# Optimization experiments

Measured on AMD Instinct MI355X. Metric: run time of the kernel, lower is better.

## Reference

```python
import jax, jax.numpy as jnp
import numpy as np
from jax import lax

V, E, H, L, T, B = 50000, 512, 1024, 2, 512, 64


def _lstm_layer(x_seq, h0, c0, W_ih, W_hh):
    # x_seq: [T, B, D_in]; W_ih: [4H, D_in]; W_hh: [4H, H]
    x_proj = jnp.einsum('tbd,gd->tbg', x_seq, W_ih)  # precompute input projection

    def step(carry, xp):
        h, c = carry
        gates = xp + h @ W_hh.T  # [B, 4H], PyTorch gate order i,f,g,o
        i, f, g, o = jnp.split(gates, 4, axis=-1)
        i = jax.nn.sigmoid(i)
        f = jax.nn.sigmoid(f)
        g = jnp.tanh(g)
        o = jax.nn.sigmoid(o)
        c = f * c + i * g
        h = o * jnp.tanh(c)
        return (h, c), h

    (hT, cT), ys = lax.scan(step, (h0, c0), x_proj)
    return ys, hT, cT


def setup_inputs() -> dict:
    key = jax.random.key(0)
    ks = jax.random.split(key, 8)
    inputs = jax.random.randint(ks[0], (T, B), 0, V)
    h0 = jnp.zeros((L, B, H), jnp.float32)
    c0 = jnp.zeros((L, B, H), jnp.float32)
    emb = jax.random.uniform(ks[1], (V, E), jnp.float32, -0.1, 0.1)
    s_ih0 = 1.0 / np.sqrt(H)
    W_ih0 = jax.random.uniform(ks[2], (4 * H, E), jnp.float32, -s_ih0, s_ih0)
    W_hh0 = jax.random.uniform(ks[3], (4 * H, H), jnp.float32, -s_ih0, s_ih0)
    W_ih1 = jax.random.uniform(ks[4], (4 * H, H), jnp.float32, -s_ih0, s_ih0)
    W_hh1 = jax.random.uniform(ks[5], (4 * H, H), jnp.float32, -s_ih0, s_ih0)
    dec_W = jax.random.uniform(ks[6], (1, H), jnp.float32, -0.1, 0.1)
    dec_b = jnp.zeros((1,), jnp.float32)
    return {"inputs": inputs, "h0": h0, "c0": c0, "emb": emb,
            "W_ih0": W_ih0, "W_hh0": W_hh0, "W_ih1": W_ih1, "W_hh1": W_hh1,
            "dec_W": dec_W, "dec_b": dec_b}


def reference(inputs, h0, c0, emb, W_ih0, W_hh0, W_ih1, W_hh1, dec_W, dec_b):
    x = emb[inputs]                                      # [T, B, E]
    y0, h1, c1 = _lstm_layer(x, h0[0], c0[0], W_ih0, W_hh0)   # [T, B, H]
    # dropout between layers is inference-disabled (eval mode)
    y1, h2, c2 = _lstm_layer(y0, h0[1], c0[1], W_ih1, W_hh1)  # [T, B, H]
    pooled = jnp.mean(y1, axis=0)                        # [B, H] (squeeze is a no-op)
    decoded = pooled @ dec_W.T + dec_b                   # [B, 1]
    hn = jnp.stack([h1, h2])
    cn = jnp.stack([c1, c2])
    return decoded, hn, cn
```

## Files before the change

kernel.cpp:

```cpp
#include <hip/hip_runtime.h>

#define TT 512
#define BB 64
#define HH 1024
#define EE 512
#define VV 50000
#define BBHH (BB*HH)
#define BPL 128
#define NBLK 256

typedef __attribute__((ext_vector_type(8))) short bf16x8;
typedef __attribute__((ext_vector_type(4))) float f32x4;

__device__ inline unsigned short f2b(float f){
  unsigned int u; __builtin_memcpy(&u, &f, 4);
  unsigned int r = (u + 0x7FFFu + ((u >> 16) & 1u)) >> 16;
  return (unsigned short)r;
}
__device__ inline float sigmoidf_(float x){ return 1.0f / (1.0f + __expf(-x)); }
__device__ inline float tanhf_(float x){ float e = __expf(2.0f * x); return 1.0f - 2.0f / (e + 1.0f); }

__device__ inline bf16x8 pack8(float4 a, float4 b){
  bf16x8 r;
  r[0] = (short)f2b(a.x); r[1] = (short)f2b(a.y); r[2] = (short)f2b(a.z); r[3] = (short)f2b(a.w);
  r[4] = (short)f2b(b.x); r[5] = (short)f2b(b.y); r[6] = (short)f2b(b.z); r[7] = (short)f2b(b.w);
  return r;
}

__global__ void cast_f2b(const float* __restrict__ src, unsigned short* __restrict__ dst, long n){
  long i = ((long)blockIdx.x * blockDim.x + threadIdx.x) * 4;
  long stride = (long)gridDim.x * blockDim.x * 4;
  for (; i + 3 < n; i += stride){
    float4 v = *reinterpret_cast<const float4*>(src + i);
    ushort4 r;
    r.x = f2b(v.x); r.y = f2b(v.y); r.z = f2b(v.z); r.w = f2b(v.w);
    *reinterpret_cast<ushort4*>(dst + i) = r;
  }
}

__global__ void init_h(const float* __restrict__ h0,
                       unsigned short* __restrict__ h0ic, unsigned short* __restrict__ h1ic){
  int i = blockIdx.x * blockDim.x + threadIdx.x;
  int b = i >> 10, j = i & (HH - 1);
  int d = (((j >> 3) * BB) + b) * 8 + (j & 7);
  h0ic[d] = f2b(h0[i]);
  h1ic[d] = f2b(h0[BBHH + i]);
}

__device__ __forceinline__ void wait_layer(const unsigned* __restrict__ f, unsigned e, int lane){
  unsigned a = __hip_atomic_load(f + lane,      __ATOMIC_RELAXED, __HIP_MEMORY_SCOPE_AGENT);
  unsigned b = __hip_atomic_load(f + 64 + lane, __ATOMIC_RELAXED, __HIP_MEMORY_SCOPE_AGENT);
  while (!__all(a >= e && b >= e)){
    __builtin_amdgcn_s_sleep(8);
    a = __hip_atomic_load(f + lane,      __ATOMIC_RELAXED, __HIP_MEMORY_SCOPE_AGENT);
    b = __hip_atomic_load(f + 64 + lane, __ATOMIC_RELAXED, __HIP_MEMORY_SCOPE_AGENT);
  }
}

__device__ __forceinline__ void publish(unsigned* __restrict__ f, int bid_l, unsigned e){
  asm volatile("s_waitcnt vmcnt(0)" ::: "memory");
  __syncthreads();
  if (threadIdx.x == 0)
    __hip_atomic_store(f + bid_l, e, __ATOMIC_RELAXED, __HIP_MEMORY_SCOPE_AGENT);
}

#define LIDX(m, s) ((((m) * 16 + (s)) * 64 + lane) * 4)

#define CBASE ((wid * 32 + hi) * (BB * 8) + l16 * 8)

__device__ void run_l0(
    int bid_l, int lane, int wid, int l16, int hi, int kq,
    const int* __restrict__ inputs, const float* __restrict__ c0,
    const unsigned short* __restrict__ emb_bf,
    const float* __restrict__ Wih0, const float* __restrict__ Whh0,
    const unsigned short* __restrict__ h0ic,
    unsigned short* __restrict__ hist0,
    float* __restrict__ hn, float* __restrict__ cn,
    unsigned* __restrict__ flags0, float* lds)
{
  const int j0 = bid_l * 8;
  const int bown = wid * 16 + l16;
  const int cbase = CBASE;

  bf16x8 wx[2][4], wh[2][8];
  #pragma unroll
  for (int m = 0; m < 2; ++m){
    const int g = l16 & 3;
    const int u = 2 * (l16 >> 2) + m;
    const float* rx = Wih0 + (size_t)(g * HH + j0 + u) * EE;
    const float* rh = Whh0 + (size_t)(g * HH + j0 + u) * HH;
    #pragma unroll
    for (int kk = 0; kk < 4; ++kk){
      int k0 = wid * 128 + kk * 32 + kq;
      wx[m][kk] = pack8(*reinterpret_cast<const float4*>(rx + k0),
                        *reinterpret_cast<const float4*>(rx + k0 + 4));
    }
    #pragma unroll
    for (int kk = 0; kk < 8; ++kk){
      int k0 = wid * 256 + kk * 32 + kq;
      wh[m][kk] = pack8(*reinterpret_cast<const float4*>(rh + k0),
                        *reinterpret_cast<const float4*>(rh + k0 + 4));
    }
  }

  float cs[2];
  #pragma unroll
  for (int m = 0; m < 2; ++m)
    cs[m] = c0[(size_t)bown * HH + j0 + 2 * hi + m];

  for (int t = 0; t < TT; ++t){
    f32x4 acc[2][4];
    #pragma unroll
    for (int m = 0; m < 2; ++m)
      #pragma unroll
      for (int nt = 0; nt < 4; ++nt)
        acc[m][nt] = (f32x4){0.f,0.f,0.f,0.f};

    {
      const unsigned short* xr[4];
      #pragma unroll
      for (int nt = 0; nt < 4; ++nt)
        xr[nt] = emb_bf + (size_t)inputs[t * BB + nt * 16 + l16] * EE;
      #pragma unroll
      for (int kk = 0; kk < 4; ++kk){
        const int kb = wid * 128 + kk * 32 + kq;
        #pragma unroll
        for (int nt = 0; nt < 4; ++nt){
          bf16x8 bf = *reinterpret_cast<const bf16x8*>(xr[nt] + kb);
          acc[0][nt] = __builtin_amdgcn_mfma_f32_16x16x32_bf16(wx[0][kk], bf, acc[0][nt], 0, 0, 0);
          acc[1][nt] = __builtin_amdgcn_mfma_f32_16x16x32_bf16(wx[1][kk], bf, acc[1][nt], 0, 0, 0);
        }
      }
    }

    if (t > 0) wait_layer(flags0, (unsigned)t, lane);

    {
      const unsigned short* hs = (t == 0) ? h0ic : hist0 + (size_t)(t - 1) * BBHH;
      #pragma unroll
      for (int kk = 0; kk < 8; ++kk){
        #pragma unroll
        for (int nt = 0; nt < 4; ++nt){
          bf16x8 bf = *reinterpret_cast<const bf16x8*>(hs + cbase + kk * 2048 + nt * 128);
          acc[0][nt] = __builtin_amdgcn_mfma_f32_16x16x32_bf16(wh[0][kk], bf, acc[0][nt], 0, 0, 0);
          acc[1][nt] = __builtin_amdgcn_mfma_f32_16x16x32_bf16(wh[1][kk], bf, acc[1][nt], 0, 0, 0);
        }
      }
    }

    #pragma unroll
    for (int m = 0; m < 2; ++m)
      #pragma unroll
      for (int nt = 0; nt < 4; ++nt)
        *reinterpret_cast<f32x4*>(&lds[LIDX(m, wid * 4 + nt)]) = acc[m][nt];
    __syncthreads();
    f32x4 s[2];
    #pragma unroll
    for (int m = 0; m < 2; ++m){
      s[m] = (f32x4){0.f,0.f,0.f,0.f};
      #pragma unroll
      for (int w = 0; w < 4; ++w)
        s[m] += *reinterpret_cast<f32x4*>(&lds[LIDX(m, w * 4 + wid)]);
    }

    float hv[2];
    #pragma unroll
    for (int m = 0; m < 2; ++m){
      float gi = sigmoidf_(s[m][0]), gf = sigmoidf_(s[m][1]);
      float gg = tanhf_(s[m][2]),    go = sigmoidf_(s[m][3]);
      cs[m] = gf * cs[m] + gi * gg;
      hv[m] = go * tanhf_(cs[m]);
    }
    unsigned w = (unsigned)f2b(hv[0]) | ((unsigned)f2b(hv[1]) << 16);
    __hip_atomic_store(reinterpret_cast<unsigned*>(hist0 + (size_t)t * BBHH + (size_t)(bid_l * BB + bown) * 8 + 2 * hi),
                       w, __ATOMIC_RELAXED, __HIP_MEMORY_SCOPE_AGENT);
    if (t == TT - 1){
      size_t o = (size_t)bown * HH + j0 + 2 * hi;
      *reinterpret_cast<float2*>(hn + o) = make_float2(hv[0], hv[1]);
      *reinterpret_cast<float2*>(cn + o) = make_float2(cs[0], cs[1]);
    }

    publish(flags0, bid_l, (unsigned)(t + 1));
  }
}

__device__ void run_l1(
    int bid_l, int lane, int wid, int l16, int hi, int kq,
    const float* __restrict__ c0,
    const float* __restrict__ Wih1, const float* __restrict__ Whh1,
    const unsigned short* __restrict__ h1ic,
    const unsigned short* __restrict__ hist0, unsigned short* __restrict__ hist1,
    const float* __restrict__ decW, const float* __restrict__ decb,
    float* __restrict__ dec_out, float* __restrict__ hn, float* __restrict__ cn,
    unsigned* __restrict__ flags0, unsigned* __restrict__ flags1, float* lds)
{
  const int j0 = bid_l * 8;
  const int bown = wid * 16 + l16;
  const int cbase = CBASE;

  bf16x8 wx[2][8], wh[2][8];
  #pragma unroll
  for (int m = 0; m < 2; ++m){
    const int g = l16 & 3;
    const int u = 2 * (l16 >> 2) + m;
    const float* rx = Wih1 + (size_t)(g * HH + j0 + u) * HH;
    const float* rh = Whh1 + (size_t)(g * HH + j0 + u) * HH;
    #pragma unroll
    for (int kk = 0; kk < 8; ++kk){
      int k0 = wid * 256 + kk * 32 + kq;
      wx[m][kk] = pack8(*reinterpret_cast<const float4*>(rx + k0),
                        *reinterpret_cast<const float4*>(rx + k0 + 4));
      wh[m][kk] = pack8(*reinterpret_cast<const float4*>(rh + k0),
                        *reinterpret_cast<const float4*>(rh + k0 + 4));
    }
  }

  float cs[2];
  #pragma unroll
  for (int m = 0; m < 2; ++m)
    cs[m] = c0[(size_t)BBHH + (size_t)bown * HH + j0 + 2 * hi + m];
  float pooldec = 0.0f;
  const float dwv0 = decW[j0 + 2 * hi], dwv1 = decW[j0 + 2 * hi + 1];

  for (int t = 0; t < TT; ++t){
    f32x4 acc[2][4];
    #pragma unroll
    for (int m = 0; m < 2; ++m)
      #pragma unroll
      for (int nt = 0; nt < 4; ++nt)
        acc[m][nt] = (f32x4){0.f,0.f,0.f,0.f};

    if (t > 0) wait_layer(flags1, (unsigned)t, lane);
    {
      const unsigned short* hs = (t == 0) ? h1ic : hist1 + (size_t)(t - 1) * BBHH;
      #pragma unroll
      for (int kk = 0; kk < 8; ++kk){
        #pragma unroll
        for (int nt = 0; nt < 4; ++nt){
          bf16x8 bf = *reinterpret_cast<const bf16x8*>(hs + cbase + kk * 2048 + nt * 128);
          acc[0][nt] = __builtin_amdgcn_mfma_f32_16x16x32_bf16(wh[0][kk], bf, acc[0][nt], 0, 0, 0);
          acc[1][nt] = __builtin_amdgcn_mfma_f32_16x16x32_bf16(wh[1][kk], bf, acc[1][nt], 0, 0, 0);
        }
      }
    }

    wait_layer(flags0, (unsigned)(t + 1), lane);
    {
      const unsigned short* xs = hist0 + (size_t)t * BBHH;
      #pragma unroll
      for (int kk = 0; kk < 8; ++kk){
        #pragma unroll
        for (int nt = 0; nt < 4; ++nt){
          bf16x8 bf = *reinterpret_cast<const bf16x8*>(xs + cbase + kk * 2048 + nt * 128);
          acc[0][nt] = __builtin_amdgcn_mfma_f32_16x16x32_bf16(wx[0][kk], bf, acc[0][nt], 0, 0, 0);
          acc[1][nt] = __builtin_amdgcn_mfma_f32_16x16x32_bf16(wx[1][kk], bf, acc[1][nt], 0, 0, 0);
        }
      }
    }

    #pragma unroll
    for (int m = 0; m < 2; ++m)
      #pragma unroll
      for (int nt = 0; nt < 4; ++nt)
        *reinterpret_cast<f32x4*>(&lds[LIDX(m, wid * 4 + nt)]) = acc[m][nt];
    __syncthreads();
    f32x4 s[2];
    #pragma unroll
    for (int m = 0; m < 2; ++m){
      s[m] = (f32x4){0.f,0.f,0.f,0.f};
      #pragma unroll
      for (int w = 0; w < 4; ++w)
        s[m] += *reinterpret_cast<f32x4*>(&lds[LIDX(m, w * 4 + wid)]);
    }

    float hv[2];
    #pragma unroll
    for (int m = 0; m < 2; ++m){
      float gi = sigmoidf_(s[m][0]), gf = sigmoidf_(s[m][1]);
      float gg = tanhf_(s[m][2]),    go = sigmoidf_(s[m][3]);
      cs[m] = gf * cs[m] + gi * gg;
      hv[m] = go * tanhf_(cs[m]);
    }
    unsigned w = (unsigned)f2b(hv[0]) | ((unsigned)f2b(hv[1]) << 16);
    __hip_atomic_store(reinterpret_cast<unsigned*>(hist1 + (size_t)t * BBHH + (size_t)(bid_l * BB + bown) * 8 + 2 * hi),
                       w, __ATOMIC_RELAXED, __HIP_MEMORY_SCOPE_AGENT);
    pooldec += hv[0] * dwv0 + hv[1] * dwv1;
    if (t == TT - 1){
      size_t o = (size_t)BBHH + (size_t)bown * HH + j0 + 2 * hi;
      *reinterpret_cast<float2*>(hn + o) = make_float2(hv[0], hv[1]);
      *reinterpret_cast<float2*>(cn + o) = make_float2(cs[0], cs[1]);
    }

    publish(flags1, bid_l, (unsigned)(t + 1));
  }

  pooldec += __shfl_xor(pooldec, 16);
  pooldec += __shfl_xor(pooldec, 32);
  if (hi == 0){
    float contrib = pooldec * (1.0f / (float)TT);
    if (bid_l == 0) contrib += decb[0];
    atomicAdd(&dec_out[bown], contrib);
  }
}

__global__ __launch_bounds__(256, 1) void lstm_persist(
    const int* __restrict__ inputs, const float* __restrict__ c0,
    const unsigned short* __restrict__ emb_bf,
    const float* __restrict__ Wih0, const float* __restrict__ Whh0,
    const float* __restrict__ Wih1, const float* __restrict__ Whh1,
    const unsigned short* __restrict__ h0ic, const unsigned short* __restrict__ h1ic,
    unsigned short* __restrict__ hist0, unsigned short* __restrict__ hist1,
    const float* __restrict__ decW, const float* __restrict__ decb,
    float* __restrict__ dec_out, float* __restrict__ hn, float* __restrict__ cn,
    unsigned* __restrict__ flags)
{
  __shared__ float lds[2 * 16 * 64 * 4];
  const int tid  = threadIdx.x;
  const int lane = tid & 63;
  const int wid  = tid >> 6;
  const int l16  = lane & 15;
  const int hi   = lane >> 4;
  const int kq   = hi << 3;
  unsigned* flags0 = flags;
  unsigned* flags1 = flags + 128;

  int bid = blockIdx.x;
  if (bid < BPL){
    run_l0(bid, lane, wid, l16, hi, kq, inputs, c0, emb_bf, Wih0, Whh0,
           h0ic, hist0, hn, cn, flags0, lds);
  } else {
    run_l1(bid - BPL, lane, wid, l16, hi, kq, c0, Wih1, Whh1,
           h1ic, hist0, hist1, decW, decb, dec_out, hn, cn, flags0, flags1, lds);
  }
}

extern "C" void kernel_launch(void* const* d_in, const int* in_sizes, int n_in,
                              void* d_out, int out_size, void* d_ws, size_t ws_size,
                              hipStream_t stream){
  const int*   inputs = (const int*)d_in[0];
  const float* h0     = (const float*)d_in[1];
  const float* c0     = (const float*)d_in[2];
  const float* emb    = (const float*)d_in[3];
  const float* Wih0   = (const float*)d_in[4];
  const float* Whh0   = (const float*)d_in[5];
  const float* Wih1   = (const float*)d_in[6];
  const float* Whh1   = (const float*)d_in[7];
  const float* decW   = (const float*)d_in[8];
  const float* decb   = (const float*)d_in[9];

  char* ws = (char*)d_ws;
  size_t off = 0;
  auto alloc = [&](size_t bytes) -> void* {
    void* p = ws + off;
    off += (bytes + 255) & ~(size_t)255;
    return p;
  };
  unsigned short* emb_bf = (unsigned short*)alloc((size_t)VV * EE * 2);
  unsigned short* hist0  = (unsigned short*)alloc((size_t)TT * BBHH * 2);
  unsigned short* hist1  = (unsigned short*)alloc((size_t)TT * BBHH * 2);
  unsigned short* h0ic   = (unsigned short*)alloc((size_t)BBHH * 2);
  unsigned short* h1ic   = (unsigned short*)alloc((size_t)BBHH * 2);
  unsigned int*   flags  = (unsigned int*)alloc((size_t)256 * 4);

  float* out = (float*)d_out;
  float* hn  = out + BB;
  float* cn  = out + BB + 2 * BBHH;

  hipMemsetAsync(flags, 0, 256 * 4, stream);
  hipMemsetAsync(out, 0, BB * 4, stream);

  cast_f2b<<<2048, 256, 0, stream>>>(emb, emb_bf, (long)VV * EE);
  init_h<<<BBHH / 256, 256, 0, stream>>>(h0, h0ic, h1ic);

  lstm_persist<<<NBLK, 256, 0, stream>>>(inputs, c0, emb_bf,
                                         Wih0, Whh0, Wih1, Whh1,
                                         h0ic, h1ic, hist0, hist1,
                                         decW, decb, out, hn, cn, flags);
}
```

Baseline: 4.286 ms.

## Split batch across 8 waves and replace block barriers with LDS counters

Doubles each persistent block to 512 threads (8 waves), splitting the batch in half across wave pairs so each wave issues half as many MFMAs per step. Block-wide __syncthreads are replaced with LDS atomic counters and a single-wave global flag poll that releases the other waves through an LDS go-word. The cross-block publish becomes a last-arriver atomic increment, which aims to shorten the per-timestep critical path. In exchange there are more waves per CU, spin loops on LDS, and more complex memory-ordering reasoning that could be fragile.

```diff
diff --git a/kernel.cpp b/kernel.cpp
--- a/kernel.cpp
+++ b/kernel.cpp
@@ -11,35 +11,38 @@
 
 typedef __attribute__((ext_vector_type(8))) short bf16x8;
 typedef __attribute__((ext_vector_type(4))) float f32x4;
-
-__device__ inline unsigned short f2b(float f){
-  unsigned int u; __builtin_memcpy(&u, &f, 4);
-  unsigned int r = (u + 0x7FFFu + ((u >> 16) & 1u)) >> 16;
-  return (unsigned short)r;
+typedef unsigned short us;
+
+#define MFMA(a,b,c) __builtin_amdgcn_mfma_f32_16x16x32_bf16((a),(b),(c),0,0,0)
+#define LDG(p) __hip_atomic_load((p), __ATOMIC_RELAXED, __HIP_MEMORY_SCOPE_AGENT)
+#define ZIDX(ks,m,ntg,ln) (((((ks)*2+(m))*4+(ntg))*64+(ln))*4)
+
+__device__ inline us f2b(float f){
+  unsigned u; __builtin_memcpy(&u, &f, 4);
+  return (us)((u + 0x7FFFu + ((u >> 16) & 1u)) >> 16);
 }
 __device__ inline float sigmoidf_(float x){ return 1.0f / (1.0f + __expf(-x)); }
 __device__ inline float tanhf_(float x){ float e = __expf(2.0f * x); return 1.0f - 2.0f / (e + 1.0f); }
 
 __device__ inline bf16x8 pack8(float4 a, float4 b){
   bf16x8 r;
-  r[0] = (short)f2b(a.x); r[1] = (short)f2b(a.y); r[2] = (short)f2b(a.z); r[3] = (short)f2b(a.w);
-  r[4] = (short)f2b(b.x); r[5] = (short)f2b(b.y); r[6] = (short)f2b(b.z); r[7] = (short)f2b(b.w);
+  r[0]=(short)f2b(a.x); r[1]=(short)f2b(a.y); r[2]=(short)f2b(a.z); r[3]=(short)f2b(a.w);
+  r[4]=(short)f2b(b.x); r[5]=(short)f2b(b.y); r[6]=(short)f2b(b.z); r[7]=(short)f2b(b.w);
   return r;
 }
 
-__global__ void cast_f2b(const float* __restrict__ src, unsigned short* __restrict__ dst, long n){
+__global__ void cast_f2b(const float* __restrict__ src, us* __restrict__ dst, long n){
   long i = ((long)blockIdx.x * blockDim.x + threadIdx.x) * 4;
   long stride = (long)gridDim.x * blockDim.x * 4;
   for (; i + 3 < n; i += stride){
     float4 v = *reinterpret_cast<const float4*>(src + i);
-    ushort4 r;
-    r.x = f2b(v.x); r.y = f2b(v.y); r.z = f2b(v.z); r.w = f2b(v.w);
+    ushort4 r; r.x=f2b(v.x); r.y=f2b(v.y); r.z=f2b(v.z); r.w=f2b(v.w);
     *reinterpret_cast<ushort4*>(dst + i) = r;
   }
 }
 
 __global__ void init_h(const float* __restrict__ h0,
-                       unsigned short* __restrict__ h0ic, unsigned short* __restrict__ h1ic){
+                       us* __restrict__ h0ic, us* __restrict__ h1ic){
   int i = blockIdx.x * blockDim.x + threadIdx.x;
   int b = i >> 10, j = i & (HH - 1);
   int d = (((j >> 3) * BB) + b) * 8 + (j & 7);
@@ -47,290 +50,326 @@
   h1ic[d] = f2b(h0[BBHH + i]);
 }
 
-__device__ __forceinline__ void wait_layer(const unsigned* __restrict__ f, unsigned e, int lane){
-  unsigned a = __hip_atomic_load(f + lane,      __ATOMIC_RELAXED, __HIP_MEMORY_SCOPE_AGENT);
-  unsigned b = __hip_atomic_load(f + 64 + lane, __ATOMIC_RELAXED, __HIP_MEMORY_SCOPE_AGENT);
-  while (!__all(a >= e && b >= e)){
-    __builtin_amdgcn_s_sleep(8);
-    a = __hip_atomic_load(f + lane,      __ATOMIC_RELAXED, __HIP_MEMORY_SCOPE_AGENT);
-    b = __hip_atomic_load(f + 64 + lane, __ATOMIC_RELAXED, __HIP_MEMORY_SCOPE_AGENT);
-  }
-}
-
-__device__ __forceinline__ void publish(unsigned* __restrict__ f, int bid_l, unsigned e){
-  asm volatile("s_waitcnt vmcnt(0)" ::: "memory");
-  __syncthreads();
-  if (threadIdx.x == 0)
-    __hip_atomic_store(f + bid_l, e, __ATOMIC_RELAXED, __HIP_MEMORY_SCOPE_AGENT);
-}
-
-#define LIDX(m, s) ((((m) * 16 + (s)) * 64 + lane) * 4)
-
-#define CBASE ((wid * 32 + hi) * (BB * 8) + l16 * 8)
-
-__device__ void run_l0(
-    int bid_l, int lane, int wid, int l16, int hi, int kq,
-    const int* __restrict__ inputs, const float* __restrict__ c0,
-    const unsigned short* __restrict__ emb_bf,
-    const float* __restrict__ Wih0, const float* __restrict__ Whh0,
-    const unsigned short* __restrict__ h0ic,
-    unsigned short* __restrict__ hist0,
+__device__ __forceinline__ void poll_flags(const unsigned* f, unsigned e, int lane){
+  for(;;){
+    unsigned a = LDG(f + lane);
+    unsigned b = LDG(f + 64 + lane);
+    if (__all((int)(a >= e && b >= e))) break;
+    __builtin_amdgcn_s_sleep(1);
+  }
+}
+__device__ __forceinline__ void wave_gate(unsigned* go, unsigned gval,
+                                          const unsigned* f, unsigned e, int lane, int wid){
+  if (wid == 0){
+    poll_flags(f, e, lane);
+    __hip_atomic_store(go, gval, __ATOMIC_RELAXED, __HIP_MEMORY_SCOPE_WORKGROUP);
+  } else {
+    while (__hip_atomic_load(go, __ATOMIC_RELAXED, __HIP_MEMORY_SCOPE_WORKGROUP) < gval)
+      __builtin_amdgcn_s_sleep(1);
+  }
+}
+__device__ __forceinline__ void lds_spin(unsigned* c, unsigned tgt){
+  while (__hip_atomic_load(c, __ATOMIC_RELAXED, __HIP_MEMORY_SCOPE_WORKGROUP) < tgt)
+    __builtin_amdgcn_s_sleep(1);
+}
+
+__device__ void run_l0(int bid_l, const int* __restrict__ inputs, const float* __restrict__ c0,
+    const us* __restrict__ emb_bf, const float* __restrict__ Wih0, const float* __restrict__ Whh0,
+    const us* __restrict__ h0ic, us* __restrict__ hist0,
     float* __restrict__ hn, float* __restrict__ cn,
-    unsigned* __restrict__ flags0, float* lds)
+    unsigned* __restrict__ flags0,
+    float* zone, unsigned* ctrA, unsigned* ctrR, unsigned* ctrP, unsigned* go0)
 {
+  const int tid = threadIdx.x, lane = tid & 63, wid = tid >> 6;
+  const int l16 = lane & 15, hi = lane >> 4, kq = hi << 3;
+  const int ks = wid & 3, bh = wid >> 2;
   const int j0 = bid_l * 8;
-  const int bown = wid * 16 + l16;
-  const int cbase = CBASE;
 
   bf16x8 wx[2][4], wh[2][8];
   #pragma unroll
   for (int m = 0; m < 2; ++m){
-    const int g = l16 & 3;
-    const int u = 2 * (l16 >> 2) + m;
+    const int g = l16 & 3, u = 2 * (l16 >> 2) + m;
     const float* rx = Wih0 + (size_t)(g * HH + j0 + u) * EE;
     const float* rh = Whh0 + (size_t)(g * HH + j0 + u) * HH;
     #pragma unroll
     for (int kk = 0; kk < 4; ++kk){
-      int k0 = wid * 128 + kk * 32 + kq;
-      wx[m][kk] = pack8(*reinterpret_cast<const float4*>(rx + k0),
-                        *reinterpret_cast<const float4*>(rx + k0 + 4));
+      int k0 = ks * 128 + kk * 32 + kq;
+      wx[m][kk] = pack8(*(const float4*)(rx + k0), *(const float4*)(rx + k0 + 4));
     }
     #pragma unroll
     for (int kk = 0; kk < 8; ++kk){
-      int k0 = wid * 256 + kk * 32 + kq;
-      wh[m][kk] = pack8(*reinterpret_cast<const float4*>(rh + k0),
-                        *reinterpret_cast<const float4*>(rh + k0 + 4));
-    }
-  }
-
-  float cs[2];
-  #pragma unroll
-  for (int m = 0; m < 2; ++m)
-    cs[m] = c0[(size_t)bown * HH + j0 + 2 * hi + m];
+      int k0 = ks * 256 + kk * 32 + kq;
+      wh[m][kk] = pack8(*(const float4*)(rh + k0), *(const float4*)(rh + k0 + 4));
+    }
+  }
+
+  const int bown  = wid * 8 + (lane >> 2);
+  const int u0    = 2 * (lane & 3);
+  const int ntg_r = bown >> 4;
+  const int lam   = (lane & 3) * 16 + (bown & 15);
+  float cs0 = 0.f, cs1 = 0.f;
+  if (lane < 32){
+    cs0 = c0[(size_t)bown * HH + j0 + u0];
+    cs1 = c0[(size_t)bown * HH + j0 + u0 + 1];
+  }
 
   for (int t = 0; t < TT; ++t){
-    f32x4 acc[2][4];
+    f32x4 acc[2][2];
+    acc[0][0]=acc[0][1]=acc[1][0]=acc[1][1]=(f32x4){0.f,0.f,0.f,0.f};
+
+    {
+      const us* xr0 = emb_bf + (size_t)inputs[t*BB + bh*32 + l16] * EE;
+      const us* xr1 = emb_bf + (size_t)inputs[t*BB + bh*32 + 16 + l16] * EE;
+      #pragma unroll
+      for (int kk = 0; kk < 4; ++kk){
+        const int kb = ks * 128 + kk * 32 + kq;
+        bf16x8 b0 = *(const bf16x8*)(xr0 + kb);
+        bf16x8 b1 = *(const bf16x8*)(xr1 + kb);
+        acc[0][0] = MFMA(wx[0][kk], b0, acc[0][0]);
+        acc[1][0] = MFMA(wx[1][kk], b0, acc[1][0]);
+        acc[0][1] = MFMA(wx[0][kk], b1, acc[0][1]);
+        acc[1][1] = MFMA(wx[1][kk], b1, acc[1][1]);
+      }
+    }
+
+    if (t > 0){
+      asm volatile("s_waitcnt vmcnt(0)" ::: "memory");
+      if (lane == 0){
+        unsigned old = atomicAdd(ctrP, 1u);
+        if (old == 8u * (unsigned)t - 1u)
+          __hip_atomic_store(flags0 + bid_l, (unsigned)t, __ATOMIC_RELAXED, __HIP_MEMORY_SCOPE_AGENT);
+      }
+    }
+
+    if (t > 0) wave_gate(go0, (unsigned)t, flags0, (unsigned)t, lane, wid);
+
+    {
+      const us* hs = (t == 0) ? h0ic : hist0 + (size_t)(t - 1) * BBHH;
+      #pragma unroll
+      for (int kk = 0; kk < 8; ++kk){
+        const us* p = hs + (size_t)(ks * 32 + kk * 4 + hi) * 512;
+        bf16x8 b0 = *(const bf16x8*)(p + (bh*32 + l16) * 8);
+        bf16x8 b1 = *(const bf16x8*)(p + (bh*32 + 16 + l16) * 8);
+        acc[0][0] = MFMA(wh[0][kk], b0, acc[0][0]);
+        acc[1][0] = MFMA(wh[1][kk], b0, acc[1][0]);
+        acc[0][1] = MFMA(wh[0][kk], b1, acc[0][1]);
+        acc[1][1] = MFMA(wh[1][kk], b1, acc[1][1]);
+      }
+    }
+
+    if (t > 0) lds_spin(ctrR, 8u * (unsigned)t);
+
     #pragma unroll
     for (int m = 0; m < 2; ++m)
       #pragma unroll
-      for (int nt = 0; nt < 4; ++nt)
-        acc[m][nt] = (f32x4){0.f,0.f,0.f,0.f};
-
-    {
-      const unsigned short* xr[4];
-      #pragma unroll
-      for (int nt = 0; nt < 4; ++nt)
-        xr[nt] = emb_bf + (size_t)inputs[t * BB + nt * 16 + l16] * EE;
-      #pragma unroll
-      for (int kk = 0; kk < 4; ++kk){
-        const int kb = wid * 128 + kk * 32 + kq;
-        #pragma unroll
-        for (int nt = 0; nt < 4; ++nt){
-          bf16x8 bf = *reinterpret_cast<const bf16x8*>(xr[nt] + kb);
-          acc[0][nt] = __builtin_amdgcn_mfma_f32_16x16x32_bf16(wx[0][kk], bf, acc[0][nt], 0, 0, 0);
-          acc[1][nt] = __builtin_amdgcn_mfma_f32_16x16x32_bf16(wx[1][kk], bf, acc[1][nt], 0, 0, 0);
-        }
-      }
-    }
-
-    if (t > 0) wait_layer(flags0, (unsigned)t, lane);
-
-    {
-      const unsigned short* hs = (t == 0) ? h0ic : hist0 + (size_t)(t - 1) * BBHH;
-      #pragma unroll
-      for (int kk = 0; kk < 8; ++kk){
-        #pragma unroll
-        for (int nt = 0; nt < 4; ++nt){
-          bf16x8 bf = *reinterpret_cast<const bf16x8*>(hs + cbase + kk * 2048 + nt * 128);
-          acc[0][nt] = __builtin_amdgcn_mfma_f32_16x16x32_bf16(wh[0][kk], bf, acc[0][nt], 0, 0, 0);
-          acc[1][nt] = __builtin_amdgcn_mfma_f32_16x16x32_bf16(wh[1][kk], bf, acc[1][nt], 0, 0, 0);
-        }
-      }
-    }
-
-    #pragma unroll
-    for (int m = 0; m < 2; ++m)
-      #pragma unroll
-      for (int nt = 0; nt < 4; ++nt)
-        *reinterpret_cast<f32x4*>(&lds[LIDX(m, wid * 4 + nt)]) = acc[m][nt];
-    __syncthreads();
-    f32x4 s[2];
-    #pragma unroll
-    for (int m = 0; m < 2; ++m){
-      s[m] = (f32x4){0.f,0.f,0.f,0.f};
-      #pragma unroll
-      for (int w = 0; w < 4; ++w)
-        s[m] += *reinterpret_cast<f32x4*>(&lds[LIDX(m, w * 4 + wid)]);
-    }
-
-    float hv[2];
-    #pragma unroll
-    for (int m = 0; m < 2; ++m){
-      float gi = sigmoidf_(s[m][0]), gf = sigmoidf_(s[m][1]);
-      float gg = tanhf_(s[m][2]),    go = sigmoidf_(s[m][3]);
-      cs[m] = gf * cs[m] + gi * gg;
-      hv[m] = go * tanhf_(cs[m]);
-    }
-    unsigned w = (unsigned)f2b(hv[0]) | ((unsigned)f2b(hv[1]) << 16);
-    __hip_atomic_store(reinterpret_cast<unsigned*>(hist0 + (size_t)t * BBHH + (size_t)(bid_l * BB + bown) * 8 + 2 * hi),
-                       w, __ATOMIC_RELAXED, __HIP_MEMORY_SCOPE_AGENT);
-    if (t == TT - 1){
-      size_t o = (size_t)bown * HH + j0 + 2 * hi;
-      *reinterpret_cast<float2*>(hn + o) = make_float2(hv[0], hv[1]);
-      *reinterpret_cast<float2*>(cn + o) = make_float2(cs[0], cs[1]);
-    }
-
-    publish(flags0, bid_l, (unsigned)(t + 1));
-  }
-}
-
-__device__ void run_l1(
-    int bid_l, int lane, int wid, int l16, int hi, int kq,
-    const float* __restrict__ c0,
+      for (int ntl = 0; ntl < 2; ++ntl)
+        *(f32x4*)&zone[ZIDX(ks, m, bh*2 + ntl, lane)] = acc[m][ntl];
+    asm volatile("s_waitcnt lgkmcnt(0)" ::: "memory");
+    if (lane == 0) atomicAdd(ctrA, 1u);
+    lds_spin(ctrA, 8u * (unsigned)(t + 1));
+
+    if (lane < 32){
+      f32x4 s0 = (f32x4){0.f,0.f,0.f,0.f}, s1 = (f32x4){0.f,0.f,0.f,0.f};
+      #pragma unroll
+      for (int kr = 0; kr < 4; ++kr){
+        s0 += *(f32x4*)&zone[ZIDX(kr, 0, ntg_r, lam)];
+        s1 += *(f32x4*)&zone[ZIDX(kr, 1, ntg_r, lam)];
+      }
+      float gi = sigmoidf_(s0[0]), gf = sigmoidf_(s0[1]);
+      float gg = tanhf_(s0[2]),    go = sigmoidf_(s0[3]);
+      cs0 = gf * cs0 + gi * gg;
+      float hv0 = go * tanhf_(cs0);
+      gi = sigmoidf_(s1[0]); gf = sigmoidf_(s1[1]);
+      gg = tanhf_(s1[2]);    go = sigmoidf_(s1[3]);
+      cs1 = gf * cs1 + gi * gg;
+      float hv1 = go * tanhf_(cs1);
+
+      unsigned w = (unsigned)f2b(hv0) | ((unsigned)f2b(hv1) << 16);
+      __hip_atomic_store((unsigned*)(hist0 + (size_t)t * BBHH + ((size_t)(bid_l*64 + bown))*8 + u0),
+                         w, __ATOMIC_RELAXED, __HIP_MEMORY_SCOPE_AGENT);
+      if (t == TT - 1){
+        size_t o = (size_t)bown * HH + j0 + u0;
+        *reinterpret_cast<float2*>(hn + o) = make_float2(hv0, hv1);
+        *reinterpret_cast<float2*>(cn + o) = make_float2(cs0, cs1);
+      }
+    }
+    asm volatile("s_waitcnt lgkmcnt(0)" ::: "memory");
+    if (lane == 0) atomicAdd(ctrR, 1u);
+  }
+
+  asm volatile("s_waitcnt vmcnt(0)" ::: "memory");
+  if (lane == 0){
+    unsigned old = atomicAdd(ctrP, 1u);
+    if (old == 8u * (unsigned)TT - 1u)
+      __hip_atomic_store(flags0 + bid_l, (unsigned)TT, __ATOMIC_RELAXED, __HIP_MEMORY_SCOPE_AGENT);
+  }
+}
+
+__device__ void run_l1(int bid_l, const float* __restrict__ c0,
     const float* __restrict__ Wih1, const float* __restrict__ Whh1,
-    const unsigned short* __restrict__ h1ic,
-    const unsigned short* __restrict__ hist0, unsigned short* __restrict__ hist1,
+    const us* __restrict__ h1ic, const us* __restrict__ hist0, us* __restrict__ hist1,
     const float* __restrict__ decW, const float* __restrict__ decb,
     float* __restrict__ dec_out, float* __restrict__ hn, float* __restrict__ cn,
-    unsigned* __restrict__ flags0, unsigned* __restrict__ flags1, float* lds)
+    unsigned* __restrict__ flags0, unsigned* __restrict__ flags1,
+    float* zone, unsigned* ctrA, unsigned* ctrR, unsigned* ctrP,
+    unsigned* go1, unsigned* go2)
 {
+  const int tid = threadIdx.x, lane = tid & 63, wid = tid >> 6;
+  const int l16 = lane & 15, hi = lane >> 4, kq = hi << 3;
+  const int ks = wid & 3, bh = wid >> 2;
   const int j0 = bid_l * 8;
-  const int bown = wid * 16 + l16;
-  const int cbase = CBASE;
 
   bf16x8 wx[2][8], wh[2][8];
   #pragma unroll
   for (int m = 0; m < 2; ++m){
-    const int g = l16 & 3;
-    const int u = 2 * (l16 >> 2) + m;
+    const int g = l16 & 3, u = 2 * (l16 >> 2) + m;
     const float* rx = Wih1 + (size_t)(g * HH + j0 + u) * HH;
     const float* rh = Whh1 + (size_t)(g * HH + j0 + u) * HH;
     #pragma unroll
     for (int kk = 0; kk < 8; ++kk){
-      int k0 = wid * 256 + kk * 32 + kq;
-      wx[m][kk] = pack8(*reinterpret_cast<const float4*>(rx + k0),
-                        *reinterpret_cast<const float4*>(rx + k0 + 4));
-      wh[m][kk] = pack8(*reinterpret_cast<const float4*>(rh + k0),
-                        *reinterpret_cast<const float4*>(rh + k0 + 4));
-    }
-  }
-
-  float cs[2];
-  #pragma unroll
-  for (int m = 0; m < 2; ++m)
-    cs[m] = c0[(size_t)BBHH + (size_t)bown * HH + j0 + 2 * hi + m];
-  float pooldec = 0.0f;
-  const float dwv0 = decW[j0 + 2 * hi], dwv1 = decW[j0 + 2 * hi + 1];
+      int k0 = ks * 256 + kk * 32 + kq;
+      wx[m][kk] = pack8(*(const float4*)(rx + k0), *(const float4*)(rx + k0 + 4));
+      wh[m][kk] = pack8(*(const float4*)(rh + k0), *(const float4*)(rh + k0 + 4));
+    }
+  }
+
+  const int bown  = wid * 8 + (lane >> 2);
+  const int u0    = 2 * (lane & 3);
+  const int ntg_r = bown >> 4;
+  const int lam   = (lane & 3) * 16 + (bown & 15);
+  float cs0 = 0.f, cs1 = 0.f, pooldec = 0.f, dw0 = 0.f, dw1 = 0.f;
+  if (lane < 32){
+    cs0 = c0[(size_t)BBHH + (size_t)bown * HH + j0 + u0];
+    cs1 = c0[(size_t)BBHH + (size_t)bown * HH + j0 + u0 + 1];
+    dw0 = decW[j0 + u0]; dw1 = decW[j0 + u0 + 1];
+  }
 
   for (int t = 0; t < TT; ++t){
-    f32x4 acc[2][4];
+    f32x4 acc[2][2];
+    acc[0][0]=acc[0][1]=acc[1][0]=acc[1][1]=(f32x4){0.f,0.f,0.f,0.f};
+
+    if (t > 0){
+      asm volatile("s_waitcnt vmcnt(0)" ::: "memory");
+      if (lane == 0){
+        unsigned old = atomicAdd(ctrP, 1u);
+        if (old == 8u * (unsigned)t - 1u)
+          __hip_atomic_store(flags1 + bid_l, (unsigned)t, __ATOMIC_RELAXED, __HIP_MEMORY_SCOPE_AGENT);
+      }
+    }
+
+    if (t > 0) wave_gate(go1, (unsigned)t, flags1, (unsigned)t, lane, wid);
+    {
+      const us* hs = (t == 0) ? h1ic : hist1 + (size_t)(t - 1) * BBHH;
+      #pragma unroll
+      for (int kk = 0; kk < 8; ++kk){
+        const us* p = hs + (size_t)(ks * 32 + kk * 4 + hi) * 512;
+        bf16x8 b0 = *(const bf16x8*)(p + (bh*32 + l16) * 8);
+        bf16x8 b1 = *(const bf16x8*)(p + (bh*32 + 16 + l16) * 8);
+        acc[0][0] = MFMA(wh[0][kk], b0, acc[0][0]);
+        acc[1][0] = MFMA(wh[1][kk], b0, acc[1][0]);
+        acc[0][1] = MFMA(wh[0][kk], b1, acc[0][1]);
+        acc[1][1] = MFMA(wh[1][kk], b1, acc[1][1]);
+      }
+    }
+
+    wave_gate(go2, (unsigned)(t + 1), flags0, (unsigned)(t + 1), lane, wid);
+
+    {
+      const us* xs = hist0 + (size_t)t * BBHH;
+      #pragma unroll
+      for (int kk = 0; kk < 8; ++kk){
+        const us* p = xs + (size_t)(ks * 32 + kk * 4 + hi) * 512;
+        bf16x8 b0 = *(const bf16x8*)(p + (bh*32 + l16) * 8);
+        bf16x8 b1 = *(const bf16x8*)(p + (bh*32 + 16 + l16) * 8);
+        acc[0][0] = MFMA(wx[0][kk], b0, acc[0][0]);
+        acc[1][0] = MFMA(wx[1][kk], b0, acc[1][0]);
+        acc[0][1] = MFMA(wx[0][kk], b1, acc[0][1]);
+        acc[1][1] = MFMA(wx[1][kk], b1, acc[1][1]);
+      }
+    }
+
+    if (t > 0) lds_spin(ctrR, 8u * (unsigned)t);
+
     #pragma unroll
     for (int m = 0; m < 2; ++m)
       #pragma unroll
-      for (int nt = 0; nt < 4; ++nt)
-        acc[m][nt] = (f32x4){0.f,0.f,0.f,0.f};
-
-    if (t > 0) wait_layer(flags1, (unsigned)t, lane);
-    {
-      const unsigned short* hs = (t == 0) ? h1ic : hist1 + (size_t)(t - 1) * BBHH;
-      #pragma unroll
-      for (int kk = 0; kk < 8; ++kk){
-        #pragma unroll
-        for (int nt = 0; nt < 4; ++nt){
-          bf16x8 bf = *reinterpret_cast<const bf16x8*>(hs + cbase + kk * 2048 + nt * 128);
-          acc[0][nt] = __builtin_amdgcn_mfma_f32_16x16x32_bf16(wh[0][kk], bf, acc[0][nt], 0, 0, 0);
-          acc[1][nt] = __builtin_amdgcn_mfma_f32_16x16x32_bf16(wh[1][kk], bf, acc[1][nt], 0, 0, 0);
-        }
-      }
-    }
-
-    wait_layer(flags0, (unsigned)(t + 1), lane);
-    {
-      const unsigned short* xs = hist0 + (size_t)t * BBHH;
-      #pragma unroll
-      for (int kk = 0; kk < 8; ++kk){
-        #pragma unroll
-        for (int nt = 0; nt < 4; ++nt){
-          bf16x8 bf = *reinterpret_cast<const bf16x8*>(xs + cbase + kk * 2048 + nt * 128);
-          acc[0][nt] = __builtin_amdgcn_mfma_f32_16x16x32_bf16(wx[0][kk], bf, acc[0][nt], 0, 0, 0);
-          acc[1][nt] = __builtin_amdgcn_mfma_f32_16x16x32_bf16(wx[1][kk], bf, acc[1][nt], 0, 0, 0);
-        }
-      }
-    }
-
-    #pragma unroll
-    for (int m = 0; m < 2; ++m)
-      #pragma unroll
-      for (int nt = 0; nt < 4; ++nt)
-        *reinterpret_cast<f32x4*>(&lds[LIDX(m, wid * 4 + nt)]) = acc[m][nt];
-    __syncthreads();
-    f32x4 s[2];
-    #pragma unroll
-    for (int m = 0; m < 2; ++m){
-      s[m] = (f32x4){0.f,0.f,0.f,0.f};
-      #pragma unroll
-      for (int w = 0; w < 4; ++w)
-        s[m] += *reinterpret_cast<f32x4*>(&lds[LIDX(m, w * 4 + wid)]);
-    }
-
-    float hv[2];
-    #pragma unroll
-    for (int m = 0; m < 2; ++m){
-      float gi = sigmoidf_(s[m][0]), gf = sigmoidf_(s[m][1]);
-      float gg = tanhf_(s[m][2]),    go = sigmoidf_(s[m][3]);
-      cs[m] = gf * cs[m] + gi * gg;
-      hv[m] = go * tanhf_(cs[m]);
-    }
-    unsigned w = (unsigned)f2b(hv[0]) | ((unsigned)f2b(hv[1]) << 16);
-    __hip_atomic_store(reinterpret_cast<unsigned*>(hist1 + (size_t)t * BBHH + (size_t)(bid_l * BB + bown) * 8 + 2 * hi),
-                       w, __ATOMIC_RELAXED, __HIP_MEMORY_SCOPE_AGENT);
-    pooldec += hv[0] * dwv0 + hv[1] * dwv1;
-    if (t == TT - 1){
-      size_t o = (size_t)BBHH + (size_t)bown * HH + j0 + 2 * hi;
-      *reinterpret_cast<float2*>(hn + o) = make_float2(hv[0], hv[1]);
-      *reinterpret_cast<float2*>(cn + o) = make_float2(cs[0], cs[1]);
-    }
-
-    publish(flags1, bid_l, (unsigned)(t + 1));
-  }
-
-  pooldec += __shfl_xor(pooldec, 16);
-  pooldec += __shfl_xor(pooldec, 32);
-  if (hi == 0){
+      for (int ntl = 0; ntl < 2; ++ntl)
+        *(f32x4*)&zone[ZIDX(ks, m, bh*2 + ntl, lane)] = acc[m][ntl];
+    asm volatile("s_waitcnt lgkmcnt(0)" ::: "memory");
+    if (lane == 0) atomicAdd(ctrA, 1u);
+    lds_spin(ctrA, 8u * (unsigned)(t + 1));
+
+    if (lane < 32){
+      f32x4 s0 = (f32x4){0.f,0.f,0.f,0.f}, s1 = (f32x4){0.f,0.f,0.f,0.f};
+      #pragma unroll
+      for (int kr = 0; kr < 4; ++kr){
+        s0 += *(f32x4*)&zone[ZIDX(kr, 0, ntg_r, lam)];
+        s1 += *(f32x4*)&zone[ZIDX(kr, 1, ntg_r, lam)];
+      }
+      float gi = sigmoidf_(s0[0]), gf = sigmoidf_(s0[1]);
+      float gg = tanhf_(s0[2]),    go = sigmoidf_(s0[3]);
+      cs0 = gf * cs0 + gi * gg;
+      float hv0 = go * tanhf_(cs0);
+      gi = sigmoidf_(s1[0]); gf = sigmoidf_(s1[1]);
+      gg = tanhf_(s1[2]);    go = sigmoidf_(s1[3]);
+      cs1 = gf * cs1 + gi * gg;
+      float hv1 = go * tanhf_(cs1);
+
+      unsigned w = (unsigned)f2b(hv0) | ((unsigned)f2b(hv1) << 16);
+      __hip_atomic_store((unsigned*)(hist1 + (size_t)t * BBHH + ((size_t)(bid_l*64 + bown))*8 + u0),
+                         w, __ATOMIC_RELAXED, __HIP_MEMORY_SCOPE_AGENT);
+      pooldec += hv0 * dw0 + hv1 * dw1;
+      if (t == TT - 1){
+        size_t o = (size_t)BBHH + (size_t)bown * HH + j0 + u0;
+        *reinterpret_cast<float2*>(hn + o) = make_float2(hv0, hv1);
+        *reinterpret_cast<float2*>(cn + o) = make_float2(cs0, cs1);
+      }
+    }
+    asm volatile("s_waitcnt lgkmcnt(0)" ::: "memory");
+    if (lane == 0) atomicAdd(ctrR, 1u);
+  }
+
+  asm volatile("s_waitcnt vmcnt(0)" ::: "memory");
+  if (lane == 0){
+    unsigned old = atomicAdd(ctrP, 1u);
+    if (old == 8u * (unsigned)TT - 1u)
+      __hip_atomic_store(flags1 + bid_l, (unsigned)TT, __ATOMIC_RELAXED, __HIP_MEMORY_SCOPE_AGENT);
+  }
+
+  pooldec += __shfl_xor(pooldec, 1);
+  pooldec += __shfl_xor(pooldec, 2);
+  if (lane < 32 && (lane & 3) == 0){
     float contrib = pooldec * (1.0f / (float)TT);
     if (bid_l == 0) contrib += decb[0];
     atomicAdd(&dec_out[bown], contrib);
   }
 }
 
-__global__ __launch_bounds__(256, 1) void lstm_persist(
+__global__ __launch_bounds__(512, 2) void lstm_persist(
     const int* __restrict__ inputs, const float* __restrict__ c0,
-    const unsigned short* __restrict__ emb_bf,
+    const us* __restrict__ emb_bf,
     const float* __restrict__ Wih0, const float* __restrict__ Whh0,
     const float* __restrict__ Wih1, const float* __restrict__ Whh1,
-    const unsigned short* __restrict__ h0ic, const unsigned short* __restrict__ h1ic,
-    unsigned short* __restrict__ hist0, unsigned short* __restrict__ hist1,
+    const us* __restrict__ h0ic, const us* __restrict__ h1ic,
+    us* __restrict__ hist0, us* __restrict__ hist1,
     const float* __restrict__ decW, const float* __restrict__ decb,
     float* __restrict__ dec_out, float* __restrict__ hn, float* __restrict__ cn,
     unsigned* __restrict__ flags)
 {
-  __shared__ float lds[2 * 16 * 64 * 4];
-  const int tid  = threadIdx.x;
-  const int lane = tid & 63;
-  const int wid  = tid >> 6;
-  const int l16  = lane & 15;
-  const int hi   = lane >> 4;
-  const int kq   = hi << 3;
+  __shared__ float zone[4*2*4*64*4];
+  __shared__ unsigned ctrA, ctrR, ctrP, goA, goB;
+  if (threadIdx.x == 0){ ctrA = 0; ctrR = 0; ctrP = 0; goA = 0; goB = 0; }
+  __syncthreads();
+
   unsigned* flags0 = flags;
   unsigned* flags1 = flags + 128;
-
   int bid = blockIdx.x;
   if (bid < BPL){
-    run_l0(bid, lane, wid, l16, hi, kq, inputs, c0, emb_bf, Wih0, Whh0,
-           h0ic, hist0, hn, cn, flags0, lds);
+    run_l0(bid, inputs, c0, emb_bf, Wih0, Whh0, h0ic, hist0, hn, cn,
+           flags0, zone, &ctrA, &ctrR, &ctrP, &goA);
   } else {
-    run_l1(bid - BPL, lane, wid, l16, hi, kq, c0, Wih1, Whh1,
-           h1ic, hist0, hist1, decW, decb, dec_out, hn, cn, flags0, flags1, lds);
+    run_l1(bid - BPL, c0, Wih1, Whh1, h1ic, hist0, hist1, decW, decb,
+           dec_out, hn, cn, flags0, flags1, zone, &ctrA, &ctrR, &ctrP, &goA, &goB);
   }
 }
 
@@ -355,12 +394,12 @@
     off += (bytes + 255) & ~(size_t)255;
     return p;
   };
-  unsigned short* emb_bf = (unsigned short*)alloc((size_t)VV * EE * 2);
-  unsigned short* hist0  = (unsigned short*)alloc((size_t)TT * BBHH * 2);
-  unsigned short* hist1  = (unsigned short*)alloc((size_t)TT * BBHH * 2);
-  unsigned short* h0ic   = (unsigned short*)alloc((size_t)BBHH * 2);
-  unsigned short* h1ic   = (unsigned short*)alloc((size_t)BBHH * 2);
-  unsigned int*   flags  = (unsigned int*)alloc((size_t)256 * 4);
+  us* emb_bf = (us*)alloc((size_t)VV * EE * 2);
+  us* hist0  = (us*)alloc((size_t)TT * BBHH * 2);
+  us* hist1  = (us*)alloc((size_t)TT * BBHH * 2);
+  us* h0ic   = (us*)alloc((size_t)BBHH * 2);
+  us* h1ic   = (us*)alloc((size_t)BBHH * 2);
+  unsigned* flags = (unsigned*)alloc((size_t)256 * 4);
 
   float* out = (float*)d_out;
   float* hn  = out + BB;
@@ -372,7 +411,7 @@
   cast_f2b<<<2048, 256, 0, stream>>>(emb, emb_bf, (long)VV * EE);
   init_h<<<BBHH / 256, 256, 0, stream>>>(h0, h0ic, h1ic);
 
-  lstm_persist<<<NBLK, 256, 0, stream>>>(inputs, c0, emb_bf,
+  lstm_persist<<<NBLK, 512, 0, stream>>>(inputs, c0, emb_bf,
                                          Wih0, Whh0, Wih1, Whh1,
                                          h0ic, h1ic, hist0, hist1,
                                          decW, decb, out, hn, cn, flags);
```

Result: slower. 5.691 ms (+32.8%).
